# Performance work log

Hardware: AMD Instinct MI355X
Metric: run time of the kernel (lower is better)

Reference implementation:

```python
import jax, jax.numpy as jnp
import numpy as np

LN_EPS = 1e-5


def setup_inputs() -> dict:
    key = jax.random.key(0)
    ks = jax.random.split(key, 6)
    B, S, D = 4, 4096, 2048
    Db = D // 4  # bottleneck_dim = n_embd // compression_ratio
    hidden = jax.random.normal(ks[0], (B, S, D), dtype=jnp.float32)
    # LayerNorm params (torch defaults: gamma=1, beta=0)
    ln_gamma = jnp.ones((D,), dtype=jnp.float32)
    ln_beta = jnp.zeros((D,), dtype=jnp.float32)
    # Linear weights, torch default init: U(-1/sqrt(fan_in), 1/sqrt(fan_in))
    bd_lim = 1.0 / np.sqrt(D)
    W_down = jax.random.uniform(ks[1], (D, Db), minval=-bd_lim, maxval=bd_lim, dtype=jnp.float32)
    b_down = jax.random.uniform(ks[2], (Db,), minval=-bd_lim, maxval=bd_lim, dtype=jnp.float32)
    bu_lim = 1.0 / np.sqrt(Db)
    W_up = jax.random.uniform(ks[3], (Db, D), minval=-bu_lim, maxval=bu_lim, dtype=jnp.float32)
    b_up = jax.random.uniform(ks[4], (D,), minval=-bu_lim, maxval=bu_lim, dtype=jnp.float32)
    alpha = jnp.array(0.01, dtype=jnp.float32)
    return {
        "hidden": hidden,
        "ln_gamma": ln_gamma,
        "ln_beta": ln_beta,
        "W_down": W_down,
        "b_down": b_down,
        "W_up": W_up,
        "b_up": b_up,
        "alpha": alpha,
        "layer_idx": 0,
    }


def reference(hidden, ln_gamma, ln_beta, W_down, b_down, W_up, b_up, alpha, layer_idx):
    # LayerNorm over last dim
    mu = jnp.mean(hidden, axis=-1, keepdims=True)
    var = jnp.mean(jnp.square(hidden - mu), axis=-1, keepdims=True)
    h_norm = (hidden - mu) * jax.lax.rsqrt(var + LN_EPS) * ln_gamma + ln_beta
    # down-proj -> SiLU -> up-proj   [b s d] @ [d k] -> [b s k] -> [b s d]
    z = jnp.einsum("bsd,dk->bsk", h_norm, W_down) + b_down
    z = jax.nn.silu(z)
    bottleneck_out = jnp.einsum("bsk,kd->bsd", z, W_up) + b_up
    # alpha-gated residual
    return hidden + alpha * (bottleneck_out - hidden)
```

## Files before the change

kernel.cpp:

```cpp
#include <hip/hip_runtime.h>

typedef __bf16 bf16x8 __attribute__((ext_vector_type(8)));
typedef __bf16 bf16x4 __attribute__((ext_vector_type(4)));
typedef float f32x4 __attribute__((ext_vector_type(4)));

__global__ __launch_bounds__(256) void prep_kernel(const float* __restrict__ Wd,
                                                   __bf16* __restrict__ Wtd,
                                                   const float* __restrict__ Wu,
                                                   __bf16* __restrict__ Wtu,
                                                   int D, int Db) {
    const float* W;
    __bf16* Wt;
    int K, N, tile;
    const int ntile_d = (Db / 32) * (D / 32);
    if ((int)blockIdx.x < ntile_d) {
        W = Wd; Wt = Wtd; K = D; N = Db; tile = blockIdx.x;
    } else {
        W = Wu; Wt = Wtu; K = Db; N = D; tile = blockIdx.x - ntile_d;
    }
    const int tn = tile % (N / 32), tk = tile / (N / 32);
    const int n0 = tn * 32, k0 = tk * 32;
    __shared__ float t[32][33];
    const int c = threadIdx.x & 31, r0 = threadIdx.x >> 5;
#pragma unroll
    for (int r = r0; r < 32; r += 8)
        t[r][c] = W[(size_t)(k0 + r) * N + n0 + c];
    __syncthreads();
#pragma unroll
    for (int r = r0; r < 32; r += 8)
        Wt[(size_t)(n0 + r) * K + k0 + c] = (__bf16)t[c][r];
}

__global__ __launch_bounds__(256) void ln_kernel(const float* __restrict__ x,
                                                 const float* __restrict__ g,
                                                 const float* __restrict__ be,
                                                 __bf16* __restrict__ y, int D) {
    const int t = threadIdx.x;
    const size_t row = blockIdx.x;
    const float4* xr = (const float4*)(x + row * (size_t)D);
    const int nv = D >> 3;
    float s = 0.f, ss = 0.f;
    for (int i = t; i < nv; i += 256) {
        float4 v0 = xr[i * 2], v1 = xr[i * 2 + 1];
        s += v0.x + v0.y + v0.z + v0.w + v1.x + v1.y + v1.z + v1.w;
        ss += v0.x * v0.x + v0.y * v0.y + v0.z * v0.z + v0.w * v0.w +
              v1.x * v1.x + v1.y * v1.y + v1.z * v1.z + v1.w * v1.w;
    }
    for (int o = 32; o > 0; o >>= 1) {
        s += __shfl_down(s, o);
        ss += __shfl_down(ss, o);
    }
    __shared__ float ps[4], pss[4], mv[2];
    int w = t >> 6;
    if ((t & 63) == 0) { ps[w] = s; pss[w] = ss; }
    __syncthreads();
    if (t == 0) {
        float S = ps[0] + ps[1] + ps[2] + ps[3];
        float SS = pss[0] + pss[1] + pss[2] + pss[3];
        float mu = S / (float)D;
        float var = SS / (float)D - mu * mu;
        mv[0] = mu;
        mv[1] = rsqrtf(var + 1e-5f);
    }
    __syncthreads();
    float mu = mv[0], rstd = mv[1];
    const float4* gg = (const float4*)g;
    const float4* bb = (const float4*)be;
    bf16x8* yr = (bf16x8*)(y + row * (size_t)D);
    for (int i = t; i < nv; i += 256) {
        float4 v0 = xr[i * 2], v1 = xr[i * 2 + 1];
        float4 g0 = gg[i * 2], g1 = gg[i * 2 + 1];
        float4 b0 = bb[i * 2], b1 = bb[i * 2 + 1];
        bf16x8 o;
        o[0] = (__bf16)((v0.x - mu) * rstd * g0.x + b0.x);
        o[1] = (__bf16)((v0.y - mu) * rstd * g0.y + b0.y);
        o[2] = (__bf16)((v0.z - mu) * rstd * g0.z + b0.z);
        o[3] = (__bf16)((v0.w - mu) * rstd * g0.w + b0.w);
        o[4] = (__bf16)((v1.x - mu) * rstd * g1.x + b1.x);
        o[5] = (__bf16)((v1.y - mu) * rstd * g1.y + b1.y);
        o[6] = (__bf16)((v1.z - mu) * rstd * g1.z + b1.z);
        o[7] = (__bf16)((v1.w - mu) * rstd * g1.w + b1.w);
        yr[i] = o;
    }
}

template <int EPI>
__global__ __launch_bounds__(256) void gemm_bt(const __bf16* __restrict__ A,
                                               const __bf16* __restrict__ Bt,
                                               const float* __restrict__ bias,
                                               const float* __restrict__ hid,
                                               const float* __restrict__ alpha_p,
                                               void* __restrict__ Cout,
                                               int M, int N, int K) {
    constexpr int BM = 128, BN = 128, BK = 32;
    __shared__ __align__(16) __bf16 Ads[BM * BK];
    __shared__ __align__(16) __bf16 Bds[BN * BK];

    const int tid = threadIdx.x;
    const int wave = tid >> 6;
    const int lane = tid & 63;
    const int bn = blockIdx.x, bm = blockIdx.y;
    const int row0 = bm * BM, col0 = bn * BN;
    const int wr = wave >> 1, wc = wave & 1;

    f32x4 acc[4][4] = {};

    const __bf16* Ag = A + (size_t)row0 * K;
    const __bf16* Bg = Bt + (size_t)col0 * K;
    const int lrow = lane >> 2;
    const int lk = (lane & 3) * 8;

    const int c = lane & 15;
    const int q = lane >> 4;

    for (int k0 = 0; k0 < K; k0 += BK) {
#pragma unroll
        for (int p = 0; p < 2; ++p) {
            int r = wave * 32 + p * 16;
            __builtin_amdgcn_global_load_lds(
                (__attribute__((address_space(1))) void*)(Ag + (size_t)(r + lrow) * K + k0 + lk),
                (__attribute__((address_space(3))) void*)(Ads + r * BK),
                16, 0, 0);
            __builtin_amdgcn_global_load_lds(
                (__attribute__((address_space(1))) void*)(Bg + (size_t)(r + lrow) * K + k0 + lk),
                (__attribute__((address_space(3))) void*)(Bds + r * BK),
                16, 0, 0);
        }
        __syncthreads();

        bf16x8 afW[4], bfA[4];
#pragma unroll
        for (int j = 0; j < 4; ++j)
            afW[j] = *(const bf16x8*)(Bds + (wc * 64 + j * 16 + c) * BK + q * 8);
#pragma unroll
        for (int i = 0; i < 4; ++i)
            bfA[i] = *(const bf16x8*)(Ads + (wr * 64 + i * 16 + c) * BK + q * 8);
#pragma unroll
        for (int i = 0; i < 4; ++i)
#pragma unroll
            for (int j = 0; j < 4; ++j)
                acc[i][j] = __builtin_amdgcn_mfma_f32_16x16x32_bf16(afW[j], bfA[i],
                                                                    acc[i][j], 0, 0, 0);
        __syncthreads();
    }

    float alpha = (EPI == 1) ? *alpha_p : 0.f;
#pragma unroll
    for (int i = 0; i < 4; ++i) {
        const int rowg = row0 + wr * 64 + i * 16 + c;
#pragma unroll
        for (int j = 0; j < 4; ++j) {
            const int colb = col0 + wc * 64 + j * 16 + q * 4;
            const float4 bv = *(const float4*)(bias + colb);
            float v0 = acc[i][j][0] + bv.x;
            float v1 = acc[i][j][1] + bv.y;
            float v2 = acc[i][j][2] + bv.z;
            float v3 = acc[i][j][3] + bv.w;
            const size_t idx = (size_t)rowg * N + colb;
            if (EPI == 0) {
                bf16x4 o;
                o[0] = (__bf16)(v0 / (1.f + __expf(-v0)));
                o[1] = (__bf16)(v1 / (1.f + __expf(-v1)));
                o[2] = (__bf16)(v2 / (1.f + __expf(-v2)));
                o[3] = (__bf16)(v3 / (1.f + __expf(-v3)));
                *(bf16x4*)((__bf16*)Cout + idx) = o;
            } else {
                const float4 h = *(const float4*)(hid + idx);
                float4 o;
                o.x = h.x + alpha * (v0 - h.x);
                o.y = h.y + alpha * (v1 - h.y);
                o.z = h.z + alpha * (v2 - h.z);
                o.w = h.w + alpha * (v3 - h.w);
                *(float4*)((float*)Cout + idx) = o;
            }
        }
    }
}

extern "C" void kernel_launch(void* const* d_in, const int* in_sizes, int n_in,
                              void* d_out, int out_size, void* d_ws, size_t ws_size,
                              hipStream_t stream) {
    const float* hidden = (const float*)d_in[0];
    const float* ln_gamma = (const float*)d_in[1];
    const float* ln_beta = (const float*)d_in[2];
    const float* W_down = (const float*)d_in[3];
    const float* b_down = (const float*)d_in[4];
    const float* W_up = (const float*)d_in[5];
    const float* b_up = (const float*)d_in[6];
    const float* alpha = (const float*)d_in[7];
    float* out = (float*)d_out;

    const int D = in_sizes[2];
    const int Db = in_sizes[4];
    const int M = in_sizes[0] / D;

    char* w = (char*)d_ws;
    __bf16* hn = (__bf16*)w;  w += (size_t)M * D * sizeof(__bf16);
    __bf16* z = (__bf16*)w;   w += (size_t)M * Db * sizeof(__bf16);
    __bf16* Wtd = (__bf16*)w; w += (size_t)D * Db * sizeof(__bf16);
    __bf16* Wtu = (__bf16*)w; w += (size_t)Db * D * sizeof(__bf16);

    const int ntiles = 2 * (D / 32) * (Db / 32);
    prep_kernel<<<ntiles, 256, 0, stream>>>(W_down, Wtd, W_up, Wtu, D, Db);

    ln_kernel<<<M, 256, 0, stream>>>(hidden, ln_gamma, ln_beta, hn, D);

    gemm_bt<0><<<dim3(Db / 128, M / 128), 256, 0, stream>>>(
        hn, Wtd, b_down, nullptr, nullptr, (void*)z, M, Db, D);

    gemm_bt<1><<<dim3(D / 128, M / 128), 256, 0, stream>>>(
        z, Wtu, b_up, hidden, alpha, (void*)out, M, D, Db);
}
```

Baseline: 395.3 us.

## Double-buffer GEMM LDS tiles with XOR swizzle and merge prep with layernorm

Fuses the weight transpose kernel and the layernorm kernel into one launch, with blocks split by index. The GEMM now double-buffers its LDS tiles: it issues the next k-slice's global-to-LDS loads before computing the current one and waits on vmcnt instead of using a full __syncthreads. An XOR swizzle on the k-chunk offset is meant to reduce LDS bank conflicts, and launch_bounds now requests 4 blocks per CU. The costs are twice the LDS per block and hand-written waitcnt and barrier sequencing, which is fragile if the compiler reorders loads.

```diff
diff --git a/kernel.cpp b/kernel.cpp
--- a/kernel.cpp
+++ b/kernel.cpp
@@ -4,39 +4,41 @@
 typedef __bf16 bf16x4 __attribute__((ext_vector_type(4)));
 typedef float f32x4 __attribute__((ext_vector_type(4)));
 
-__global__ __launch_bounds__(256) void prep_kernel(const float* __restrict__ Wd,
-                                                   __bf16* __restrict__ Wtd,
-                                                   const float* __restrict__ Wu,
-                                                   __bf16* __restrict__ Wtu,
-                                                   int D, int Db) {
-    const float* W;
-    __bf16* Wt;
-    int K, N, tile;
-    const int ntile_d = (Db / 32) * (D / 32);
-    if ((int)blockIdx.x < ntile_d) {
-        W = Wd; Wt = Wtd; K = D; N = Db; tile = blockIdx.x;
-    } else {
-        W = Wu; Wt = Wtu; K = Db; N = D; tile = blockIdx.x - ntile_d;
-    }
-    const int tn = tile % (N / 32), tk = tile / (N / 32);
-    const int n0 = tn * 32, k0 = tk * 32;
-    __shared__ float t[32][33];
-    const int c = threadIdx.x & 31, r0 = threadIdx.x >> 5;
-#pragma unroll
-    for (int r = r0; r < 32; r += 8)
-        t[r][c] = W[(size_t)(k0 + r) * N + n0 + c];
-    __syncthreads();
-#pragma unroll
-    for (int r = r0; r < 32; r += 8)
-        Wt[(size_t)(n0 + r) * K + k0 + c] = (__bf16)t[c][r];
-}
-
-__global__ __launch_bounds__(256) void ln_kernel(const float* __restrict__ x,
-                                                 const float* __restrict__ g,
-                                                 const float* __restrict__ be,
-                                                 __bf16* __restrict__ y, int D) {
+#define S_BARRIER() asm volatile("s_barrier" ::: "memory")
+#define WAITCNT_VM(n) asm volatile("s_waitcnt vmcnt(" #n ")" ::: "memory")
+#define WAITCNT_LGKM0() asm volatile("s_waitcnt lgkmcnt(0)" ::: "memory")
+
+__global__ __launch_bounds__(256) void prep_ln_kernel(
+    const float* __restrict__ Wd, __bf16* __restrict__ Wtd,
+    const float* __restrict__ Wu, __bf16* __restrict__ Wtu,
+    const float* __restrict__ x, const float* __restrict__ g,
+    const float* __restrict__ be, __bf16* __restrict__ y,
+    int D, int Db, int ntiles) {
+    if ((int)blockIdx.x < ntiles) {
+        const float* W;
+        __bf16* Wt;
+        int K, N, tile;
+        const int ntile_d = (Db / 32) * (D / 32);
+        if ((int)blockIdx.x < ntile_d) {
+            W = Wd; Wt = Wtd; K = D; N = Db; tile = blockIdx.x;
+        } else {
+            W = Wu; Wt = Wtu; K = Db; N = D; tile = blockIdx.x - ntile_d;
+        }
+        const int tn = tile % (N / 32), tk = tile / (N / 32);
+        const int n0 = tn * 32, k0 = tk * 32;
+        __shared__ float t[32][33];
+        const int c = threadIdx.x & 31, r0 = threadIdx.x >> 5;
+#pragma unroll
+        for (int r = r0; r < 32; r += 8)
+            t[r][c] = W[(size_t)(k0 + r) * N + n0 + c];
+        __syncthreads();
+#pragma unroll
+        for (int r = r0; r < 32; r += 8)
+            Wt[(size_t)(n0 + r) * K + k0 + c] = (__bf16)t[c][r];
+        return;
+    }
     const int t = threadIdx.x;
-    const size_t row = blockIdx.x;
+    const size_t row = blockIdx.x - ntiles;
     const float4* xr = (const float4*)(x + row * (size_t)D);
     const int nv = D >> 3;
     float s = 0.f, ss = 0.f;
@@ -85,16 +87,16 @@
 }
 
 template <int EPI>
-__global__ __launch_bounds__(256) void gemm_bt(const __bf16* __restrict__ A,
-                                               const __bf16* __restrict__ Bt,
-                                               const float* __restrict__ bias,
-                                               const float* __restrict__ hid,
-                                               const float* __restrict__ alpha_p,
-                                               void* __restrict__ Cout,
-                                               int M, int N, int K) {
+__global__ __launch_bounds__(256, 4) void gemm_bt(const __bf16* __restrict__ A,
+                                                  const __bf16* __restrict__ Bt,
+                                                  const float* __restrict__ bias,
+                                                  const float* __restrict__ hid,
+                                                  const float* __restrict__ alpha_p,
+                                                  void* __restrict__ Cout,
+                                                  int M, int N, int K) {
     constexpr int BM = 128, BN = 128, BK = 32;
-    __shared__ __align__(16) __bf16 Ads[BM * BK];
-    __shared__ __align__(16) __bf16 Bds[BN * BK];
+    __shared__ __align__(16) __bf16 Ads[2][BM * BK];
+    __shared__ __align__(16) __bf16 Bds[2][BN * BK];
 
     const int tid = threadIdx.x;
     const int wave = tid >> 6;
@@ -108,40 +110,57 @@
     const __bf16* Ag = A + (size_t)row0 * K;
     const __bf16* Bg = Bt + (size_t)col0 * K;
     const int lrow = lane >> 2;
-    const int lk = (lane & 3) * 8;
+    const int lk = ((lane & 3) ^ (lrow & 3)) * 8;
 
     const int c = lane & 15;
     const int q = lane >> 4;
 
-    for (int k0 = 0; k0 < K; k0 += BK) {
+    auto stage = [&](int k0, int b) {
 #pragma unroll
         for (int p = 0; p < 2; ++p) {
-            int r = wave * 32 + p * 16;
+            const int r = wave * 32 + p * 16;
             __builtin_amdgcn_global_load_lds(
                 (__attribute__((address_space(1))) void*)(Ag + (size_t)(r + lrow) * K + k0 + lk),
-                (__attribute__((address_space(3))) void*)(Ads + r * BK),
+                (__attribute__((address_space(3))) void*)(&Ads[b][r * BK]),
                 16, 0, 0);
             __builtin_amdgcn_global_load_lds(
                 (__attribute__((address_space(1))) void*)(Bg + (size_t)(r + lrow) * K + k0 + lk),
-                (__attribute__((address_space(3))) void*)(Bds + r * BK),
+                (__attribute__((address_space(3))) void*)(&Bds[b][r * BK]),
                 16, 0, 0);
         }
-        __syncthreads();
+    };
+
+    const int nk = K / BK;
+    stage(0, 0);
+    for (int it = 0; it < nk; ++it) {
+        const int cur = it & 1;
+        if (it + 1 < nk) {
+            stage((it + 1) * BK, cur ^ 1);
+            WAITCNT_VM(4);
+        } else {
+            WAITCNT_VM(0);
+        }
+        S_BARRIER();
 
         bf16x8 afW[4], bfA[4];
 #pragma unroll
-        for (int j = 0; j < 4; ++j)
-            afW[j] = *(const bf16x8*)(Bds + (wc * 64 + j * 16 + c) * BK + q * 8);
-#pragma unroll
-        for (int i = 0; i < 4; ++i)
-            bfA[i] = *(const bf16x8*)(Ads + (wr * 64 + i * 16 + c) * BK + q * 8);
+        for (int j = 0; j < 4; ++j) {
+            const int rl = wc * 64 + j * 16 + c;
+            afW[j] = *(const bf16x8*)(&Bds[cur][rl * BK + ((q ^ (c & 3)) * 8)]);
+        }
+#pragma unroll
+        for (int i = 0; i < 4; ++i) {
+            const int rl = wr * 64 + i * 16 + c;
+            bfA[i] = *(const bf16x8*)(&Ads[cur][rl * BK + ((q ^ (c & 3)) * 8)]);
+        }
 #pragma unroll
         for (int i = 0; i < 4; ++i)
 #pragma unroll
             for (int j = 0; j < 4; ++j)
                 acc[i][j] = __builtin_amdgcn_mfma_f32_16x16x32_bf16(afW[j], bfA[i],
                                                                     acc[i][j], 0, 0, 0);
-        __syncthreads();
+        WAITCNT_LGKM0();
+        S_BARRIER();
     }
 
     float alpha = (EPI == 1) ? *alpha_p : 0.f;
@@ -201,9 +220,9 @@
     __bf16* Wtu = (__bf16*)w; w += (size_t)Db * D * sizeof(__bf16);
 
     const int ntiles = 2 * (D / 32) * (Db / 32);
-    prep_kernel<<<ntiles, 256, 0, stream>>>(W_down, Wtd, W_up, Wtu, D, Db);
-
-    ln_kernel<<<M, 256, 0, stream>>>(hidden, ln_gamma, ln_beta, hn, D);
+    prep_ln_kernel<<<ntiles + M, 256, 0, stream>>>(W_down, Wtd, W_up, Wtu,
+                                                   hidden, ln_gamma, ln_beta, hn,
+                                                   D, Db, ntiles);
 
     gemm_bt<0><<<dim3(Db / 128, M / 128), 256, 0, stream>>>(
         hn, Wtd, b_down, nullptr, nullptr, (void*)z, M, Db, D);
```

Result: no change. 394.3 us (-0.2%).
